# Performance work log

Hardware: AMD Instinct MI355X
Metric: run time of the kernel (lower is better)

Reference implementation:

```python
import jax, jax.numpy as jnp
import numpy as np

CANVAS = 28
MARGIN = 2
HALF = CANVAS / 2.0          # 14
SCALE = CANVAS / 2.0 - MARGIN  # 12
P = 2        # num_paths
SEG = 4      # final segments
T = 8        # curve samples per bezier segment
AA = 2       # 2x2 = 4 anti-alias subsamples per pixel


def _lin(x, w, b):
    return x @ w + b


def _render(cp, widths, alphas):
    """diffvg-style rasterizer.
    cp: [B,P,S,4,2] cubic bezier control points, widths/alphas: [B,P].
    Returns [B,1,H,W] image over white background (paths paint dark).
    """
    B = cp.shape[0]
    t = jnp.linspace(0.0, 1.0, T)
    mt = 1.0 - t
    basis = jnp.stack([mt**3, 3*mt**2*t, 3*mt*t**2, t**3], axis=1)  # [T,4]
    pts = jnp.einsum('tk,bpskd->bpstd', basis, cp)                   # [B,P,S,T,2]
    q = pts.reshape(B, P, SEG * T, 2)                                # polyline [B,P,M,2]

    # 2x2 subpixel sample grid over the canvas
    Nf = CANVAS * AA
    c = (jnp.arange(Nf, dtype=jnp.float32) + 0.5) / AA               # fine coords
    sy, sx = jnp.meshgrid(c, c, indexing='ij')
    s = jnp.stack([sx.ravel(), sy.ravel()], axis=-1)                 # [Ns,2] (x,y)

    # stroke coverage: distance from each sample to nearest curve sample
    qq = jnp.sum(q * q, axis=-1)                                     # [B,P,M]
    ss = jnp.sum(s * s, axis=-1)                                     # [Ns]
    cr = jnp.einsum('bpmd,nd->bpmn', q, s)                           # [B,P,M,Ns]
    d2 = jnp.maximum(qq[..., None] + ss - 2.0 * cr, 0.0)
    dist = jnp.sqrt(jnp.min(d2, axis=2))                             # [B,P,Ns]
    stroke = jnp.clip(widths[..., None] * 0.5 + 0.5 - dist, 0.0, 1.0)

    # fill coverage: even-odd crossing number on the closed polyline
    qn = jnp.roll(q, -1, axis=2)
    x0, y0 = q[..., 0], q[..., 1]
    x1, y1 = qn[..., 0], qn[..., 1]
    syf, sxf = s[:, 1], s[:, 0]
    crossing_band = (y0[..., None] > syf) != (y1[..., None] > syf)   # [B,P,M,Ns]
    te = (syf - y0[..., None]) / (y1[..., None] - y0[..., None] + 1e-8)
    xint = x0[..., None] + te * (x1 - x0)[..., None]
    ncross = jnp.sum((crossing_band & (sxf < xint)).astype(jnp.int32), axis=2)
    inside = (ncross % 2).astype(dist.dtype)                         # [B,P,Ns]

    cov = jnp.maximum(inside, stroke)
    img = jnp.prod(1.0 - alphas[..., None] * cov, axis=1)            # composite over paths, bg=1
    img = img.reshape(B, CANVAS, AA, CANVAS, AA).mean(axis=(2, 4))   # AA resolve
    return img[:, None]                                              # [B,1,H,W]


def setup_inputs() -> dict:
    key = jax.random.key(0)
    ks = jax.random.split(key, 16)
    def W(k, i, o):
        return jax.random.normal(k, (i, o), jnp.float32) / np.sqrt(i).astype(np.float32)
    B = 128
    return {
        'x': jax.random.uniform(ks[0], (B, 1, 28, 28), jnp.float32),
        'eps': jax.random.normal(ks[1], (B, 64), jnp.float32),
        'enc_w1': W(ks[2], 784, 256), 'enc_b1': jnp.zeros((256,), jnp.float32),
        'enc_w2': W(ks[3], 256, 256), 'enc_b2': jnp.zeros((256,), jnp.float32),
        'mu_w': W(ks[4], 256, 64), 'mu_b': jnp.zeros((64,), jnp.float32),
        'lv_w': W(ks[5], 256, 64), 'lv_b': jnp.zeros((64,), jnp.float32),
        'dec_w1': W(ks[6], 64, 512), 'dec_b1': jnp.zeros((512,), jnp.float32),
        'dec_w2': W(ks[7], 512, 512), 'dec_b2': jnp.zeros((512,), jnp.float32),
        'cp_w': W(ks[8], 512, 28), 'cp_b': jnp.zeros((28,), jnp.float32),
        'ref_w1': W(ks[9], 92, 512), 'ref_b1': jnp.zeros((512,), jnp.float32),
        'ref_w2': W(ks[10], 512, 52), 'ref_b2': jnp.zeros((52,), jnp.float32),
        'wd_w': W(ks[11], 512, 2), 'wd_b': jnp.zeros((2,), jnp.float32),
        'al_w': W(ks[12], 512, 2), 'al_b': jnp.zeros((2,), jnp.float32),
    }


def reference(x, eps, enc_w1, enc_b1, enc_w2, enc_b2, mu_w, mu_b, lv_w, lv_b,
              dec_w1, dec_b1, dec_w2, dec_b2, cp_w, cp_b,
              ref_w1, ref_b1, ref_w2, ref_b2, wd_w, wd_b, al_w, al_b):
    B = x.shape[0]
    # encoder
    h = jax.nn.leaky_relu(_lin(x.reshape(B, -1), enc_w1, enc_b1), 0.2)
    h = jax.nn.leaky_relu(_lin(h, enc_w2, enc_b2), 0.2)
    mu = _lin(h, mu_w, mu_b)
    logvar = _lin(h, lv_w, lv_b)
    z = mu + eps * jnp.exp(0.5 * logvar)
    # hierarchical decoder
    h2 = jax.nn.selu(_lin(jax.nn.selu(_lin(z, dec_w1, dec_b1)), dec_w2, dec_b2))
    coarse = jnp.tanh(_lin(h2, cp_w, cp_b)).reshape(B, P, 7, 2) * SCALE + HALF
    pts_norm = (coarse - HALF) / SCALE
    h_in = jnp.concatenate([z, pts_norm.reshape(B, -1)], axis=-1)
    refined = jnp.tanh(_lin(jax.nn.selu(_lin(h_in, ref_w1, ref_b1)), ref_w2, ref_b2))
    points = refined.reshape(B, P, 13, 2) * SCALE + HALF
    seg_idx = 3 * jnp.arange(SEG)[:, None] + jnp.arange(4)[None, :]  # [S,4]
    control_points = points[:, :, seg_idx, :]                         # [B,P,S,4,2]
    widths = jax.nn.sigmoid(_lin(h2, wd_w, wd_b)) * 2.0 + 1.0
    alphas = jax.nn.sigmoid(_lin(h2, al_w, al_b))
    rendered = 1.0 - _render(control_points, widths, alphas)          # white digit on black
    return (rendered, mu, logvar, control_points, widths, alphas)
```

## Files before the change

### kernel.cpp

```cpp
#include <hip/hip_runtime.h>
#include <math.h>


#define O_MU  100352
#define O_LV  108544
#define O_CP  116736
#define O_WD  124928
#define O_AL  125184

__device__ __forceinline__ float leaky(float x) {
    return x >= 0.0f ? x : 0.2f * x;
}
__device__ __forceinline__ float selu(float x) {
    const float scale = 1.0507009873554805f;
    const float alpha = 1.6732632423543772f;
    return x > 0.0f ? scale * x : scale * (alpha * expm1f(x));
}
__device__ __forceinline__ void fma4(float4& acc, float a, const float4 w) {
    acc.x = fmaf(a, w.x, acc.x);
    acc.y = fmaf(a, w.y, acc.y);
    acc.z = fmaf(a, w.z, acc.z);
    acc.w = fmaf(a, w.w, acc.w);
}
__device__ __forceinline__ void add4(float4& a, const float4 b) {
    a.x += b.x; a.y += b.y; a.z += b.z; a.w += b.w;
}

__global__ __launch_bounds__(512, 1)
void pipeline(const float* __restrict__ x, const float* __restrict__ eps,
              const float* __restrict__ enc_w1, const float* __restrict__ enc_b1,
              const float* __restrict__ enc_w2, const float* __restrict__ enc_b2,
              const float* __restrict__ mu_w, const float* __restrict__ mu_b,
              const float* __restrict__ lv_w, const float* __restrict__ lv_b,
              const float* __restrict__ dec_w1, const float* __restrict__ dec_b1,
              const float* __restrict__ dec_w2, const float* __restrict__ dec_b2,
              const float* __restrict__ cp_w, const float* __restrict__ cp_b,
              const float* __restrict__ ref_w1, const float* __restrict__ ref_b1,
              const float* __restrict__ ref_w2, const float* __restrict__ ref_b2,
              const float* __restrict__ wd_w, const float* __restrict__ wd_b,
              const float* __restrict__ al_w, const float* __restrict__ al_b,
              float* __restrict__ out) {
    __shared__ float  sX[784];
    __shared__ float4 sPart4[512];
    __shared__ float  sH1[256];
    __shared__ float  sHe[256];
    __shared__ float  sML[128];
    __shared__ float  sIn[96];
    __shared__ float  sD1[512];
    __shared__ float  sH2[512];
    __shared__ float  sR1[512];
    __shared__ float  sP[56];
    __shared__ float  sQ[128];
    __shared__ float  sWA[4];

    const int row = blockIdx.x;
    const int tid = threadIdx.x;

    for (int i = tid; i < 784; i += 512) sX[i] = x[row * 784 + i];
    __syncthreads();

    {
        const int jv = tid & 63, g = tid >> 6;
        const float4* __restrict__ W4 = (const float4*)enc_w1;
        const int k0 = g * 98;
        float4 acc0 = {0,0,0,0}, acc1 = {0,0,0,0};
#pragma unroll 7
        for (int i = 0; i < 98; i += 2) {
            fma4(acc0, sX[k0 + i + 0], W4[(k0 + i + 0) * 64 + jv]);
            fma4(acc1, sX[k0 + i + 1], W4[(k0 + i + 1) * 64 + jv]);
        }
        add4(acc0, acc1);
        sPart4[g * 64 + jv] = acc0;
    }
    __syncthreads();
    if (tid < 64) {
        float4 s = ((const float4*)enc_b1)[tid];
#pragma unroll
        for (int g = 0; g < 8; g++) add4(s, sPart4[g * 64 + tid]);
        s.x = leaky(s.x); s.y = leaky(s.y); s.z = leaky(s.z); s.w = leaky(s.w);
        ((float4*)sH1)[tid] = s;
    }
    __syncthreads();

    {
        const int jv = tid & 63, g = tid >> 6;
        const float4* __restrict__ W4 = (const float4*)enc_w2;
        const int k0 = g * 32;
        float4 acc0 = {0,0,0,0}, acc1 = {0,0,0,0};
#pragma unroll 8
        for (int i = 0; i < 32; i += 2) {
            fma4(acc0, sH1[k0 + i + 0], W4[(k0 + i + 0) * 64 + jv]);
            fma4(acc1, sH1[k0 + i + 1], W4[(k0 + i + 1) * 64 + jv]);
        }
        add4(acc0, acc1);
        sPart4[g * 64 + jv] = acc0;
    }
    __syncthreads();
    if (tid < 64) {
        float4 s = ((const float4*)enc_b2)[tid];
#pragma unroll
        for (int g = 0; g < 8; g++) add4(s, sPart4[g * 64 + tid]);
        s.x = leaky(s.x); s.y = leaky(s.y); s.z = leaky(s.z); s.w = leaky(s.w);
        ((float4*)sHe)[tid] = s;
    }
    __syncthreads();

    {
        const int o4 = tid >> 4, g = tid & 15;
        const int jv = o4 & 15;
        const float4* __restrict__ W4 = (const float4*)(o4 < 16 ? mu_w : lv_w);
        const int k0 = g * 16;
        float4 acc = {0,0,0,0};
#pragma unroll
        for (int i = 0; i < 16; i++)
            fma4(acc, sHe[k0 + i], W4[(k0 + i) * 16 + jv]);
        sPart4[o4 * 16 + g] = acc;
    }
    __syncthreads();
    if (tid < 32) {
        const int jv = tid & 15;
        float4 s = (tid < 16) ? ((const float4*)mu_b)[jv] : ((const float4*)lv_b)[jv];
#pragma unroll
        for (int g = 0; g < 16; g++) add4(s, sPart4[tid * 16 + g]);
        ((float4*)sML)[tid] = s;
        float4* o4p = (float4*)(out + (tid < 16 ? O_MU : O_LV) + row * 64);
        o4p[jv] = s;
    }
    __syncthreads();
    if (tid < 64)
        sIn[tid] = fmaf(eps[row * 64 + tid], expf(0.5f * sML[64 + tid]), sML[tid]);
    __syncthreads();

    {
        const int jv = tid & 127, g = tid >> 7;
        const float4* __restrict__ W4 = (const float4*)dec_w1;
        const int k0 = g * 16;
        float4 acc = {0,0,0,0};
#pragma unroll
        for (int i = 0; i < 16; i++)
            fma4(acc, sIn[k0 + i], W4[(k0 + i) * 128 + jv]);
        sPart4[g * 128 + jv] = acc;
    }
    __syncthreads();
    if (tid < 128) {
        float4 s = ((const float4*)dec_b1)[tid];
#pragma unroll
        for (int g = 0; g < 4; g++) add4(s, sPart4[g * 128 + tid]);
        s.x = selu(s.x); s.y = selu(s.y); s.z = selu(s.z); s.w = selu(s.w);
        ((float4*)sD1)[tid] = s;
    }
    __syncthreads();

    {
        const int jv = tid & 127, g = tid >> 7;
        const float4* __restrict__ W4 = (const float4*)dec_w2;
        const int k0 = g * 128;
        float4 acc0 = {0,0,0,0}, acc1 = {0,0,0,0};
        float4 acc2 = {0,0,0,0}, acc3 = {0,0,0,0};
#pragma unroll 4
        for (int i = 0; i < 128; i += 4) {
            fma4(acc0, sD1[k0 + i + 0], W4[(k0 + i + 0) * 128 + jv]);
            fma4(acc1, sD1[k0 + i + 1], W4[(k0 + i + 1) * 128 + jv]);
            fma4(acc2, sD1[k0 + i + 2], W4[(k0 + i + 2) * 128 + jv]);
            fma4(acc3, sD1[k0 + i + 3], W4[(k0 + i + 3) * 128 + jv]);
        }
        add4(acc0, acc1); add4(acc2, acc3); add4(acc0, acc2);
        sPart4[g * 128 + jv] = acc0;
    }
    __syncthreads();
    if (tid < 128) {
        float4 s = ((const float4*)dec_b2)[tid];
#pragma unroll
        for (int g = 0; g < 4; g++) add4(s, sPart4[g * 128 + tid]);
        s.x = selu(s.x); s.y = selu(s.y); s.z = selu(s.z); s.w = selu(s.w);
        ((float4*)sH2)[tid] = s;
    }
    __syncthreads();

    {
        const int o = tid >> 4, g = tid & 15;
        const float* __restrict__ W;
        int ldw, col;
        if (o < 28)      { W = cp_w; ldw = 28; col = o; }
        else if (o < 30) { W = wd_w; ldw = 2;  col = o - 28; }
        else             { W = al_w; ldw = 2;  col = o - 30; }
        float acc = 0.f;
        for (int k = g; k < 512; k += 16) acc = fmaf(sH2[k], W[k * ldw + col], acc);
        acc += __shfl_xor(acc, 1);
        acc += __shfl_xor(acc, 2);
        acc += __shfl_xor(acc, 4);
        acc += __shfl_xor(acc, 8);
        if (g == 0) {
            if (o < 28) {
                sIn[64 + o] = tanhf(acc + cp_b[col]);
            } else if (o < 30) {
                float v = 1.f / (1.f + expf(-(acc + wd_b[col])));
                v = fmaf(v, 2.f, 1.f);
                out[O_WD + row * 2 + col] = v;
                sWA[col] = v;
            } else {
                float v = 1.f / (1.f + expf(-(acc + al_b[col])));
                out[O_AL + row * 2 + col] = v;
                sWA[2 + col] = v;
            }
        }
    }
    __syncthreads();

    {
        const int jv = tid & 127, g = tid >> 7;
        const float4* __restrict__ W4 = (const float4*)ref_w1;
        const int k0 = g * 23;
        float4 acc = {0,0,0,0};
#pragma unroll
        for (int i = 0; i < 23; i++)
            fma4(acc, sIn[k0 + i], W4[(k0 + i) * 128 + jv]);
        sPart4[g * 128 + jv] = acc;
    }
    __syncthreads();
    if (tid < 128) {
        float4 s = ((const float4*)ref_b1)[tid];
#pragma unroll
        for (int g = 0; g < 4; g++) add4(s, sPart4[g * 128 + tid]);
        s.x = selu(s.x); s.y = selu(s.y); s.z = selu(s.z); s.w = selu(s.w);
        ((float4*)sR1)[tid] = s;
    }
    __syncthreads();

    {
        const int o = tid >> 3, g = tid & 7;
        float acc = 0.f;
        if (o < 52)
            for (int k = g; k < 512; k += 8) acc = fmaf(sR1[k], ref_w2[k * 52 + o], acc);
        acc += __shfl_xor(acc, 1);
        acc += __shfl_xor(acc, 2);
        acc += __shfl_xor(acc, 4);
        if (g == 0 && o < 52)
            sP[o] = fmaf(tanhf(acc + ref_b2[o]), 12.f, 14.f);
    }
    __syncthreads();

    if (tid < 64) {
        int idx = tid;
        int p = idx >> 5, rest = idx & 31;
        int s = rest >> 3, kk = (rest >> 1) & 3, d = idx & 1;
        out[O_CP + row * 64 + idx] = sP[p * 26 + (3 * s + kk) * 2 + d];
    }
    if (tid < 128) {
        int idx = tid;
        int p = idx >> 6, s = (idx >> 4) & 3, ti = (idx >> 1) & 7, d = idx & 1;
        float t = (float)ti / 7.0f;
        float mt = 1.0f - t;
        float c0 = mt * mt * mt;
        float c1 = 3.f * mt * mt * t;
        float c2 = 3.f * mt * t * t;
        float c3 = t * t * t;
        const float* base = sP + p * 26 + (3 * s) * 2 + d;
        sQ[idx] = c0 * base[0] + c1 * base[2] + c2 * base[4] + c3 * base[6];
    }
    __syncthreads();

    const float2* __restrict__ sQ2 = (const float2*)sQ;
    for (int u = tid; u < 3136; u += 512) {
        const int pixel = u >> 2;
        const int sub = u & 3;
        const int py = pixel / 28;
        const int px = pixel - py * 28;
        const float sy = ((float)(2 * py + (sub >> 1)) + 0.5f) * 0.5f;
        const float sx = ((float)(2 * px + (sub & 1)) + 0.5f) * 0.5f;
        float img = 1.0f;
#pragma unroll
        for (int p = 0; p < 2; p++) {
            float dmin2 = 1e30f;
            int cnt = 0;
            float2 cur = sQ2[p * 32];
            bool bp = cur.y > sy;
#pragma unroll
            for (int m = 0; m < 32; m++) {
                float2 nxt = sQ2[p * 32 + ((m + 1) & 31)];
                float dx = sx - cur.x;
                float dy = sy - cur.y;
                dmin2 = fminf(dmin2, fmaf(dx, dx, dy * dy));
                bool bn = nxt.y > sy;
                float den = nxt.y - cur.y + 1e-8f;
                float lhs = dx * den;
                float rhs = dy * (nxt.x - cur.x);
                if ((bp != bn) && ((lhs < rhs) == (den > 0.0f))) cnt++;
                cur = nxt;
                bp = bn;
            }
            float dist = sqrtf(dmin2);
            float stroke = fminf(fmaxf(fmaf(sWA[p], 0.5f, 0.5f) - dist, 0.f), 1.f);
            float cov = fmaxf((float)(cnt & 1), stroke);
            img *= fmaf(-sWA[2 + p], cov, 1.0f);
        }
        img += __shfl_xor(img, 1);
        img += __shfl_xor(img, 2);
        if (sub == 0) out[row * 784 + pixel] = 1.0f - 0.25f * img;
    }
}

extern "C" void kernel_launch(void* const* d_in, const int* in_sizes, int n_in,
                              void* d_out, int out_size, void* d_ws, size_t ws_size,
                              hipStream_t stream) {
    const float* x      = (const float*)d_in[0];
    const float* eps    = (const float*)d_in[1];
    const float* enc_w1 = (const float*)d_in[2];
    const float* enc_b1 = (const float*)d_in[3];
    const float* enc_w2 = (const float*)d_in[4];
    const float* enc_b2 = (const float*)d_in[5];
    const float* mu_w   = (const float*)d_in[6];
    const float* mu_b   = (const float*)d_in[7];
    const float* lv_w   = (const float*)d_in[8];
    const float* lv_b   = (const float*)d_in[9];
    const float* dec_w1 = (const float*)d_in[10];
    const float* dec_b1 = (const float*)d_in[11];
    const float* dec_w2 = (const float*)d_in[12];
    const float* dec_b2 = (const float*)d_in[13];
    const float* cp_w   = (const float*)d_in[14];
    const float* cp_b   = (const float*)d_in[15];
    const float* ref_w1 = (const float*)d_in[16];
    const float* ref_b1 = (const float*)d_in[17];
    const float* ref_w2 = (const float*)d_in[18];
    const float* ref_b2 = (const float*)d_in[19];
    const float* wd_w   = (const float*)d_in[20];
    const float* wd_b   = (const float*)d_in[21];
    const float* al_w   = (const float*)d_in[22];
    const float* al_b   = (const float*)d_in[23];

    float* out = (float*)d_out;

    pipeline<<<128, 512, 0, stream>>>(x, eps, enc_w1, enc_b1, enc_w2, enc_b2,
                                      mu_w, mu_b, lv_w, lv_b, dec_w1, dec_b1,
                                      dec_w2, dec_b2, cp_w, cp_b, ref_w1, ref_b1,
                                      ref_w2, ref_b2, wd_w, wd_b, al_w, al_b,
                                      out);
}
```

Measured before the change: 209.8 us.

## Convert weights to fp16 in a pre-pass and stream half-precision weights in MLP

Adds a conversion kernel that writes every MLP weight matrix as fp16 into a workspace on each call. The main pipeline kernel then reads 8 halves per 16-byte load and accumulates in fp32, halving the weight bytes fetched by each of the 128 blocks. The k-split and column mapping are re-tiled to match, and the partial-sum buffer doubles in size. In exchange, the extra launch and the full fp32 read plus fp16 write of all weights are added on every call, and weight precision drops to fp16.

```diff
diff --git a/kernel.cpp b/kernel.cpp
--- a/kernel.cpp
+++ b/kernel.cpp
@@ -1,4 +1,5 @@
 #include <hip/hip_runtime.h>
+#include <hip/hip_fp16.h>
 #include <math.h>
 
 
@@ -8,6 +9,18 @@
 #define O_WD  124928
 #define O_AL  125184
 
+#define H_ENC1 0
+#define H_ENC2 200704
+#define H_MU   266240
+#define H_LV   282624
+#define H_DEC1 299008
+#define H_DEC2 331776
+#define H_CPW  593920
+#define H_REF1 608256
+#define H_REF2 655360
+#define H_WDW  681984
+#define H_ALW  683008
+
 __device__ __forceinline__ float leaky(float x) {
     return x >= 0.0f ? x : 0.2f * x;
 }
@@ -16,42 +29,79 @@
     const float alpha = 1.6732632423543772f;
     return x > 0.0f ? scale * x : scale * (alpha * expm1f(x));
 }
-__device__ __forceinline__ void fma4(float4& acc, float a, const float4 w) {
-    acc.x = fmaf(a, w.x, acc.x);
-    acc.y = fmaf(a, w.y, acc.y);
-    acc.z = fmaf(a, w.z, acc.z);
-    acc.w = fmaf(a, w.w, acc.w);
+
+struct __align__(16) H8 { __half2 h[4]; };
+
+__device__ __forceinline__ void fma8(float4& p0, float4& p1, float a, const H8& u) {
+    float2 f0 = __half22float2(u.h[0]);
+    float2 f1 = __half22float2(u.h[1]);
+    float2 f2 = __half22float2(u.h[2]);
+    float2 f3 = __half22float2(u.h[3]);
+    p0.x = fmaf(a, f0.x, p0.x); p0.y = fmaf(a, f0.y, p0.y);
+    p0.z = fmaf(a, f1.x, p0.z); p0.w = fmaf(a, f1.y, p0.w);
+    p1.x = fmaf(a, f2.x, p1.x); p1.y = fmaf(a, f2.y, p1.y);
+    p1.z = fmaf(a, f3.x, p1.z); p1.w = fmaf(a, f3.y, p1.w);
 }
 __device__ __forceinline__ void add4(float4& a, const float4 b) {
     a.x += b.x; a.y += b.y; a.z += b.z; a.w += b.w;
 }
 
+__device__ __forceinline__ void conv_arr(const float* __restrict__ s,
+                                         __half2* __restrict__ d2,
+                                         int n4, int t, int NT) {
+    const float4* __restrict__ s4 = (const float4*)s;
+    for (int i = t; i < n4; i += NT) {
+        float4 v = s4[i];
+        __half2 a; a.x = __float2half_rn(v.x); a.y = __float2half_rn(v.y);
+        __half2 b; b.x = __float2half_rn(v.z); b.y = __float2half_rn(v.w);
+        d2[2 * i] = a; d2[2 * i + 1] = b;
+    }
+}
+
+__global__ __launch_bounds__(256)
+void convert_w(const float* __restrict__ enc_w1, const float* __restrict__ enc_w2,
+               const float* __restrict__ mu_w, const float* __restrict__ lv_w,
+               const float* __restrict__ dec_w1, const float* __restrict__ dec_w2,
+               const float* __restrict__ cp_w, const float* __restrict__ ref_w1,
+               const float* __restrict__ ref_w2, const float* __restrict__ wd_w,
+               const float* __restrict__ al_w, __half* __restrict__ wh) {
+    const int t = blockIdx.x * 256 + threadIdx.x;
+    const int NT = gridDim.x * 256;
+    conv_arr(enc_w1, (__half2*)(wh + H_ENC1), 200704 / 4, t, NT);
+    conv_arr(enc_w2, (__half2*)(wh + H_ENC2), 65536 / 4, t, NT);
+    conv_arr(mu_w,   (__half2*)(wh + H_MU),   16384 / 4, t, NT);
+    conv_arr(lv_w,   (__half2*)(wh + H_LV),   16384 / 4, t, NT);
+    conv_arr(dec_w1, (__half2*)(wh + H_DEC1), 32768 / 4, t, NT);
+    conv_arr(dec_w2, (__half2*)(wh + H_DEC2), 262144 / 4, t, NT);
+    conv_arr(cp_w,   (__half2*)(wh + H_CPW),  14336 / 4, t, NT);
+    conv_arr(ref_w1, (__half2*)(wh + H_REF1), 47104 / 4, t, NT);
+    conv_arr(ref_w2, (__half2*)(wh + H_REF2), 26624 / 4, t, NT);
+    conv_arr(wd_w,   (__half2*)(wh + H_WDW),  1024 / 4, t, NT);
+    conv_arr(al_w,   (__half2*)(wh + H_ALW),  1024 / 4, t, NT);
+}
+
 __global__ __launch_bounds__(512, 1)
 void pipeline(const float* __restrict__ x, const float* __restrict__ eps,
-              const float* __restrict__ enc_w1, const float* __restrict__ enc_b1,
-              const float* __restrict__ enc_w2, const float* __restrict__ enc_b2,
-              const float* __restrict__ mu_w, const float* __restrict__ mu_b,
-              const float* __restrict__ lv_w, const float* __restrict__ lv_b,
-              const float* __restrict__ dec_w1, const float* __restrict__ dec_b1,
-              const float* __restrict__ dec_w2, const float* __restrict__ dec_b2,
-              const float* __restrict__ cp_w, const float* __restrict__ cp_b,
-              const float* __restrict__ ref_w1, const float* __restrict__ ref_b1,
-              const float* __restrict__ ref_w2, const float* __restrict__ ref_b2,
-              const float* __restrict__ wd_w, const float* __restrict__ wd_b,
-              const float* __restrict__ al_w, const float* __restrict__ al_b,
+              const __half* __restrict__ wh,
+              const float* __restrict__ enc_b1, const float* __restrict__ enc_b2,
+              const float* __restrict__ mu_b, const float* __restrict__ lv_b,
+              const float* __restrict__ dec_b1, const float* __restrict__ dec_b2,
+              const float* __restrict__ cp_b, const float* __restrict__ ref_b1,
+              const float* __restrict__ ref_b2, const float* __restrict__ wd_b,
+              const float* __restrict__ al_b,
               float* __restrict__ out) {
-    __shared__ float  sX[784];
-    __shared__ float4 sPart4[512];
-    __shared__ float  sH1[256];
-    __shared__ float  sHe[256];
-    __shared__ float  sML[128];
-    __shared__ float  sIn[96];
-    __shared__ float  sD1[512];
-    __shared__ float  sH2[512];
-    __shared__ float  sR1[512];
-    __shared__ float  sP[56];
-    __shared__ float  sQ[128];
-    __shared__ float  sWA[4];
+    __shared__            float4 sPart4[1024];
+    __shared__ __align__(16) float sX[784];
+    __shared__ __align__(16) float sH1[256];
+    __shared__ __align__(16) float sHe[256];
+    __shared__ __align__(16) float sML[128];
+    __shared__ __align__(16) float sIn[96];
+    __shared__ __align__(16) float sD1[512];
+    __shared__ __align__(16) float sH2[512];
+    __shared__ __align__(16) float sR1[512];
+    __shared__ __align__(16) float sP[56];
+    __shared__ __align__(16) float sQ[128];
+    __shared__            float sWA[4];
 
     const int row = blockIdx.x;
     const int tid = threadIdx.x;
@@ -60,71 +110,68 @@
     __syncthreads();
 
     {
-        const int jv = tid & 63, g = tid >> 6;
-        const float4* __restrict__ W4 = (const float4*)enc_w1;
-        const int k0 = g * 98;
-        float4 acc0 = {0,0,0,0}, acc1 = {0,0,0,0};
-#pragma unroll 7
-        for (int i = 0; i < 98; i += 2) {
-            fma4(acc0, sX[k0 + i + 0], W4[(k0 + i + 0) * 64 + jv]);
-            fma4(acc1, sX[k0 + i + 1], W4[(k0 + i + 1) * 64 + jv]);
-        }
-        add4(acc0, acc1);
-        sPart4[g * 64 + jv] = acc0;
+        const int jc = tid & 31, gi = tid >> 5;
+        const H8* __restrict__ W8 = (const H8*)(wh + H_ENC1);
+        const int k0 = gi * 49;
+        float4 p0 = {0,0,0,0}, p1 = {0,0,0,0};
+        for (int i = 0; i < 49; i++)
+            fma8(p0, p1, sX[k0 + i], W8[(k0 + i) * 32 + jc]);
+        sPart4[gi * 64 + jc * 2 + 0] = p0;
+        sPart4[gi * 64 + jc * 2 + 1] = p1;
     }
     __syncthreads();
     if (tid < 64) {
         float4 s = ((const float4*)enc_b1)[tid];
 #pragma unroll
-        for (int g = 0; g < 8; g++) add4(s, sPart4[g * 64 + tid]);
+        for (int g = 0; g < 16; g++) add4(s, sPart4[g * 64 + tid]);
         s.x = leaky(s.x); s.y = leaky(s.y); s.z = leaky(s.z); s.w = leaky(s.w);
         ((float4*)sH1)[tid] = s;
     }
     __syncthreads();
 
     {
-        const int jv = tid & 63, g = tid >> 6;
-        const float4* __restrict__ W4 = (const float4*)enc_w2;
-        const int k0 = g * 32;
-        float4 acc0 = {0,0,0,0}, acc1 = {0,0,0,0};
-#pragma unroll 8
-        for (int i = 0; i < 32; i += 2) {
-            fma4(acc0, sH1[k0 + i + 0], W4[(k0 + i + 0) * 64 + jv]);
-            fma4(acc1, sH1[k0 + i + 1], W4[(k0 + i + 1) * 64 + jv]);
-        }
-        add4(acc0, acc1);
-        sPart4[g * 64 + jv] = acc0;
+        const int jc = tid & 31, gi = tid >> 5;
+        const H8* __restrict__ W8 = (const H8*)(wh + H_ENC2);
+        const int k0 = gi * 16;
+        float4 p0 = {0,0,0,0}, p1 = {0,0,0,0};
+#pragma unroll
+        for (int i = 0; i < 16; i++)
+            fma8(p0, p1, sH1[k0 + i], W8[(k0 + i) * 32 + jc]);
+        sPart4[gi * 64 + jc * 2 + 0] = p0;
+        sPart4[gi * 64 + jc * 2 + 1] = p1;
     }
     __syncthreads();
     if (tid < 64) {
         float4 s = ((const float4*)enc_b2)[tid];
 #pragma unroll
-        for (int g = 0; g < 8; g++) add4(s, sPart4[g * 64 + tid]);
+        for (int g = 0; g < 16; g++) add4(s, sPart4[g * 64 + tid]);
         s.x = leaky(s.x); s.y = leaky(s.y); s.z = leaky(s.z); s.w = leaky(s.w);
         ((float4*)sHe)[tid] = s;
     }
     __syncthreads();
 
     {
-        const int o4 = tid >> 4, g = tid & 15;
-        const int jv = o4 & 15;
-        const float4* __restrict__ W4 = (const float4*)(o4 < 16 ? mu_w : lv_w);
-        const int k0 = g * 16;
-        float4 acc = {0,0,0,0};
-#pragma unroll
-        for (int i = 0; i < 16; i++)
-            fma4(acc, sHe[k0 + i], W4[(k0 + i) * 16 + jv]);
-        sPart4[o4 * 16 + g] = acc;
+        const int o8 = tid >> 5, gi = tid & 31;
+        const bool is_lv = o8 >= 8;
+        const H8* __restrict__ W8 = (const H8*)(wh + (is_lv ? H_LV : H_MU));
+        const int colu = o8 & 7;
+        const int k0 = gi * 8;
+        float4 p0 = {0,0,0,0}, p1 = {0,0,0,0};
+#pragma unroll
+        for (int i = 0; i < 8; i++)
+            fma8(p0, p1, sHe[k0 + i], W8[(k0 + i) * 8 + colu]);
+        sPart4[gi * 32 + o8 * 2 + 0] = p0;
+        sPart4[gi * 32 + o8 * 2 + 1] = p1;
     }
     __syncthreads();
     if (tid < 32) {
+        const bool is_lv = tid >= 16;
         const int jv = tid & 15;
-        float4 s = (tid < 16) ? ((const float4*)mu_b)[jv] : ((const float4*)lv_b)[jv];
-#pragma unroll
-        for (int g = 0; g < 16; g++) add4(s, sPart4[tid * 16 + g]);
+        float4 s = is_lv ? ((const float4*)lv_b)[jv] : ((const float4*)mu_b)[jv];
+#pragma unroll
+        for (int g = 0; g < 32; g++) add4(s, sPart4[g * 32 + tid]);
         ((float4*)sML)[tid] = s;
-        float4* o4p = (float4*)(out + (tid < 16 ? O_MU : O_LV) + row * 64);
-        o4p[jv] = s;
+        ((float4*)(out + (is_lv ? O_LV : O_MU) + row * 64))[jv] = s;
     }
     __syncthreads();
     if (tid < 64)
@@ -132,46 +179,42 @@
     __syncthreads();
 
     {
-        const int jv = tid & 127, g = tid >> 7;
-        const float4* __restrict__ W4 = (const float4*)dec_w1;
-        const int k0 = g * 16;
-        float4 acc = {0,0,0,0};
-#pragma unroll
-        for (int i = 0; i < 16; i++)
-            fma4(acc, sIn[k0 + i], W4[(k0 + i) * 128 + jv]);
-        sPart4[g * 128 + jv] = acc;
+        const int jc = tid & 63, gi = tid >> 6;
+        const H8* __restrict__ W8 = (const H8*)(wh + H_DEC1);
+        const int k0 = gi * 8;
+        float4 p0 = {0,0,0,0}, p1 = {0,0,0,0};
+#pragma unroll
+        for (int i = 0; i < 8; i++)
+            fma8(p0, p1, sIn[k0 + i], W8[(k0 + i) * 64 + jc]);
+        sPart4[gi * 128 + jc * 2 + 0] = p0;
+        sPart4[gi * 128 + jc * 2 + 1] = p1;
     }
     __syncthreads();
     if (tid < 128) {
         float4 s = ((const float4*)dec_b1)[tid];
 #pragma unroll
-        for (int g = 0; g < 4; g++) add4(s, sPart4[g * 128 + tid]);
+        for (int g = 0; g < 8; g++) add4(s, sPart4[g * 128 + tid]);
         s.x = selu(s.x); s.y = selu(s.y); s.z = selu(s.z); s.w = selu(s.w);
         ((float4*)sD1)[tid] = s;
     }
     __syncthreads();
 
     {
-        const int jv = tid & 127, g = tid >> 7;
-        const float4* __restrict__ W4 = (const float4*)dec_w2;
-        const int k0 = g * 128;
-        float4 acc0 = {0,0,0,0}, acc1 = {0,0,0,0};
-        float4 acc2 = {0,0,0,0}, acc3 = {0,0,0,0};
-#pragma unroll 4
-        for (int i = 0; i < 128; i += 4) {
-            fma4(acc0, sD1[k0 + i + 0], W4[(k0 + i + 0) * 128 + jv]);
-            fma4(acc1, sD1[k0 + i + 1], W4[(k0 + i + 1) * 128 + jv]);
-            fma4(acc2, sD1[k0 + i + 2], W4[(k0 + i + 2) * 128 + jv]);
-            fma4(acc3, sD1[k0 + i + 3], W4[(k0 + i + 3) * 128 + jv]);
-        }
-        add4(acc0, acc1); add4(acc2, acc3); add4(acc0, acc2);
-        sPart4[g * 128 + jv] = acc0;
+        const int jc = tid & 63, gi = tid >> 6;
+        const H8* __restrict__ W8 = (const H8*)(wh + H_DEC2);
+        const int k0 = gi * 64;
+        float4 p0 = {0,0,0,0}, p1 = {0,0,0,0};
+#pragma unroll 8
+        for (int i = 0; i < 64; i++)
+            fma8(p0, p1, sD1[k0 + i], W8[(k0 + i) * 64 + jc]);
+        sPart4[gi * 128 + jc * 2 + 0] = p0;
+        sPart4[gi * 128 + jc * 2 + 1] = p1;
     }
     __syncthreads();
     if (tid < 128) {
         float4 s = ((const float4*)dec_b2)[tid];
 #pragma unroll
-        for (int g = 0; g < 4; g++) add4(s, sPart4[g * 128 + tid]);
+        for (int g = 0; g < 8; g++) add4(s, sPart4[g * 128 + tid]);
         s.x = selu(s.x); s.y = selu(s.y); s.z = selu(s.z); s.w = selu(s.w);
         ((float4*)sH2)[tid] = s;
     }
@@ -179,13 +222,14 @@
 
     {
         const int o = tid >> 4, g = tid & 15;
-        const float* __restrict__ W;
+        const __half* __restrict__ W;
         int ldw, col;
-        if (o < 28)      { W = cp_w; ldw = 28; col = o; }
-        else if (o < 30) { W = wd_w; ldw = 2;  col = o - 28; }
-        else             { W = al_w; ldw = 2;  col = o - 30; }
+        if (o < 28)      { W = wh + H_CPW; ldw = 28; col = o; }
+        else if (o < 30) { W = wh + H_WDW; ldw = 2;  col = o - 28; }
+        else             { W = wh + H_ALW; ldw = 2;  col = o - 30; }
         float acc = 0.f;
-        for (int k = g; k < 512; k += 16) acc = fmaf(sH2[k], W[k * ldw + col], acc);
+        for (int k = g; k < 512; k += 16)
+            acc = fmaf(sH2[k], __half2float(W[k * ldw + col]), acc);
         acc += __shfl_xor(acc, 1);
         acc += __shfl_xor(acc, 2);
         acc += __shfl_xor(acc, 4);
@@ -208,20 +252,20 @@
     __syncthreads();
 
     {
-        const int jv = tid & 127, g = tid >> 7;
-        const float4* __restrict__ W4 = (const float4*)ref_w1;
-        const int k0 = g * 23;
-        float4 acc = {0,0,0,0};
-#pragma unroll
-        for (int i = 0; i < 23; i++)
-            fma4(acc, sIn[k0 + i], W4[(k0 + i) * 128 + jv]);
-        sPart4[g * 128 + jv] = acc;
+        const int jc = tid & 63, gi = tid >> 6;
+        const H8* __restrict__ W8 = (const H8*)(wh + H_REF1);
+        const int k0 = (92 * gi) >> 3, k1 = (92 * (gi + 1)) >> 3;
+        float4 p0 = {0,0,0,0}, p1 = {0,0,0,0};
+        for (int k = k0; k < k1; k++)
+            fma8(p0, p1, sIn[k], W8[k * 64 + jc]);
+        sPart4[gi * 128 + jc * 2 + 0] = p0;
+        sPart4[gi * 128 + jc * 2 + 1] = p1;
     }
     __syncthreads();
     if (tid < 128) {
         float4 s = ((const float4*)ref_b1)[tid];
 #pragma unroll
-        for (int g = 0; g < 4; g++) add4(s, sPart4[g * 128 + tid]);
+        for (int g = 0; g < 8; g++) add4(s, sPart4[g * 128 + tid]);
         s.x = selu(s.x); s.y = selu(s.y); s.z = selu(s.z); s.w = selu(s.w);
         ((float4*)sR1)[tid] = s;
     }
@@ -229,9 +273,11 @@
 
     {
         const int o = tid >> 3, g = tid & 7;
+        const __half* __restrict__ W = wh + H_REF2;
         float acc = 0.f;
         if (o < 52)
-            for (int k = g; k < 512; k += 8) acc = fmaf(sR1[k], ref_w2[k * 52 + o], acc);
+            for (int k = g; k < 512; k += 8)
+                acc = fmaf(sR1[k], __half2float(W[k * 52 + o]), acc);
         acc += __shfl_xor(acc, 1);
         acc += __shfl_xor(acc, 2);
         acc += __shfl_xor(acc, 4);
@@ -328,11 +374,13 @@
     const float* al_w   = (const float*)d_in[22];
     const float* al_b   = (const float*)d_in[23];
 
-    float* out = (float*)d_out;
-
-    pipeline<<<128, 512, 0, stream>>>(x, eps, enc_w1, enc_b1, enc_w2, enc_b2,
-                                      mu_w, mu_b, lv_w, lv_b, dec_w1, dec_b1,
-                                      dec_w2, dec_b2, cp_w, cp_b, ref_w1, ref_b1,
-                                      ref_w2, ref_b2, wd_w, wd_b, al_w, al_b,
-                                      out);
-}
+    float*  out = (float*)d_out;
+    __half* wh  = (__half*)d_ws;
+
+    convert_w<<<256, 256, 0, stream>>>(enc_w1, enc_w2, mu_w, lv_w, dec_w1,
+                                       dec_w2, cp_w, ref_w1, ref_w2, wd_w,
+                                       al_w, wh);
+    pipeline<<<128, 512, 0, stream>>>(x, eps, wh, enc_b1, enc_b2, mu_b, lv_b,
+                                      dec_b1, dec_b2, cp_b, ref_b1, ref_b2,
+                                      wd_b, al_b, out);
+}
```

Measured after the change: 210.3 us. No clear change (+0.2%).
